# Kernel tuning notes

Hardware: AMD Instinct MI355X
Metric: run time of the kernel (lower is better)

## Reference

```python
import jax, jax.numpy as jnp
import numpy as np

BATCH = 2_000_000
IN_DIM = 10
OUT_DIM = 3


def setup_inputs() -> dict:
    key = jax.random.key(0)
    kx, kw, km = jax.random.split(key, 3)
    x = jax.random.normal(kx, (BATCH, IN_DIM), dtype=jnp.float32)
    W = jax.random.normal(kw, (OUT_DIM, IN_DIM), dtype=jnp.float32)
    # M initialized near identity (well-conditioned), matching torch.eye init
    M = jnp.eye(OUT_DIM, dtype=jnp.float32) + 0.1 * jax.random.normal(km, (OUT_DIM, OUT_DIM), dtype=jnp.float32)
    return {"x": x, "W": W, "M": M}


def reference(x, W, M):
    det_A = jnp.linalg.det(M)
    is_singular = jnp.isclose(det_A, jnp.float32(0.0))  # torch.isclose defaults: rtol=1e-5, atol=1e-8
    M_inv = jnp.linalg.inv(M)
    M_inv = jnp.where(is_singular, jnp.full_like(M_inv, jnp.nan), M_inv)
    # y = (M_inv @ W @ x.T).T == x @ (M_inv @ W).T
    proj = M_inv @ W                      # [out, in] tiny matmul
    return x @ proj.T                     # [batch, out]
```

## Files before the change

kernel.cpp:

```cpp
#include <hip/hip_runtime.h>

#define IN_DIM 10
#define OUT_DIM 3
#define BLOCK 256
#define ROWS_PER_BLOCK 512

__global__ __launch_bounds__(BLOCK) void simnet_fused(
    const float* __restrict__ x,
    const float* __restrict__ W,
    const float* __restrict__ M,
    float* __restrict__ out,
    long long batch)
{
    __shared__ float s_x[ROWS_PER_BLOCK * IN_DIM];
    __shared__ float s_proj[OUT_DIM * IN_DIM];

    const int t = threadIdx.x;
    const long long row0 = (long long)blockIdx.x * ROWS_PER_BLOCK;
    const long long total_in = batch * IN_DIM;

    if (t == 0) {
        const float a = M[0], b = M[1], c = M[2];
        const float d = M[3], e = M[4], f_ = M[5];
        const float g = M[6], h = M[7], i_ = M[8];
        const float A =  (e * i_ - f_ * h);
        const float B = -(d * i_ - f_ * g);
        const float C =  (d * h  - e  * g);
        const float det = a * A + b * B + c * C;
        float inv[3][3];
        if (fabsf(det) <= 1e-8f) {
            const float qn = __builtin_nanf("");
            #pragma unroll
            for (int o = 0; o < 3; ++o)
                #pragma unroll
                for (int k = 0; k < 3; ++k) inv[o][k] = qn;
        } else {
            const float r = 1.0f / det;
            inv[0][0] = A * r;
            inv[0][1] = (c * h  - b * i_) * r;
            inv[0][2] = (b * f_ - c * e ) * r;
            inv[1][0] = B * r;
            inv[1][1] = (a * i_ - c * g ) * r;
            inv[1][2] = (c * d  - a * f_) * r;
            inv[2][0] = C * r;
            inv[2][1] = (b * g  - a * h ) * r;
            inv[2][2] = (a * e  - b * d ) * r;
        }
        #pragma unroll
        for (int o = 0; o < OUT_DIM; ++o)
            #pragma unroll
            for (int j = 0; j < IN_DIM; ++j)
                s_proj[o * IN_DIM + j] = inv[o][0] * W[0 * IN_DIM + j]
                                       + inv[o][1] * W[1 * IN_DIM + j]
                                       + inv[o][2] * W[2 * IN_DIM + j];
    }

    {
        const long long base = row0 * IN_DIM;
        #pragma unroll
        for (int k = 0; k < 5; ++k) {
            const long long f = base + (long long)(k * BLOCK + t) * 4;
            float4 v = make_float4(0.f, 0.f, 0.f, 0.f);
            if (f + 4 <= total_in) {
                v = *reinterpret_cast<const float4*>(x + f);
            } else if (f < total_in) {
                const float* p = x + f;
                const int n = (int)(total_in - f);
                v.x = p[0];
                if (n > 1) v.y = p[1];
                if (n > 2) v.z = p[2];
            }
            *reinterpret_cast<float4*>(&s_x[(k * BLOCK + t) * 4]) = v;
        }
    }
    __syncthreads();

    float pj[OUT_DIM][IN_DIM];
    #pragma unroll
    for (int o = 0; o < OUT_DIM; ++o)
        #pragma unroll
        for (int j = 0; j < IN_DIM; ++j)
            pj[o][j] = s_proj[o * IN_DIM + j];

    float acc[2][OUT_DIM];
    #pragma unroll
    for (int r = 0; r < 2; ++r) {
        const int lr = t + r * BLOCK;
        float xv[IN_DIM];
        #pragma unroll
        for (int j = 0; j < IN_DIM; ++j) xv[j] = s_x[lr * IN_DIM + j];
        #pragma unroll
        for (int o = 0; o < OUT_DIM; ++o) {
            float s = 0.f;
            #pragma unroll
            for (int j = 0; j < IN_DIM; ++j) s = fmaf(xv[j], pj[o][j], s);
            acc[r][o] = s;
        }
    }
    __syncthreads();

    #pragma unroll
    for (int r = 0; r < 2; ++r) {
        const int lr = t + r * BLOCK;
        #pragma unroll
        for (int o = 0; o < OUT_DIM; ++o)
            s_x[lr * OUT_DIM + o] = acc[r][o];
    }
    __syncthreads();

    const long long out_base = row0 * OUT_DIM;
    const long long total_out = batch * OUT_DIM;
    #pragma unroll
    for (int k = 0; k < 2; ++k) {
        const int idx = k * BLOCK + t;
        if (idx < (ROWS_PER_BLOCK * OUT_DIM) / 4) {
            const long long f = out_base + (long long)idx * 4;
            if (f + 4 <= total_out) {
                *reinterpret_cast<float4*>(out + f) =
                    *reinterpret_cast<const float4*>(&s_x[idx * 4]);
            } else if (f < total_out) {
                const int n = (int)(total_out - f);
                for (int j = 0; j < n; ++j) out[f + j] = s_x[idx * 4 + j];
            }
        }
    }
}

extern "C" void kernel_launch(void* const* d_in, const int* in_sizes, int n_in,
                              void* d_out, int out_size, void* d_ws, size_t ws_size,
                              hipStream_t stream) {
    const float* x = (const float*)d_in[0];
    const float* W = (const float*)d_in[1];
    const float* M = (const float*)d_in[2];
    float* out = (float*)d_out;
    const long long batch = (long long)in_sizes[0] / IN_DIM;
    const int grid = (int)((batch + ROWS_PER_BLOCK - 1) / ROWS_PER_BLOCK);
    simnet_fused<<<grid, BLOCK, 0, stream>>>(x, W, M, out, batch);
}
```

Measured before the change: 24.23 us.

## Split projection setup into its own kernel and make streaming kernel wave-local

```diff
diff --git a/kernel.cpp b/kernel.cpp
--- a/kernel.cpp
+++ b/kernel.cpp
@@ -3,124 +3,132 @@
 #define IN_DIM 10
 #define OUT_DIM 3
 #define BLOCK 256
-#define ROWS_PER_BLOCK 512
+#define WPB 4
+#define RPW 128
 
-__global__ __launch_bounds__(BLOCK) void simnet_fused(
+__global__ void proj_setup_kernel(const float* __restrict__ W,
+                                  const float* __restrict__ M,
+                                  float* __restrict__ proj)
+{
+    const int t = threadIdx.x;
+    const float a = M[0], b = M[1], c = M[2];
+    const float d = M[3], e = M[4], f_ = M[5];
+    const float g = M[6], h = M[7], i_ = M[8];
+    const float A =  (e * i_ - f_ * h);
+    const float B = -(d * i_ - f_ * g);
+    const float C =  (d * h  - e  * g);
+    const float det = a * A + b * B + c * C;
+    float inv[3][3];
+    if (fabsf(det) <= 1e-8f) {
+        const float qn = __builtin_nanf("");
+        #pragma unroll
+        for (int o = 0; o < 3; ++o)
+            #pragma unroll
+            for (int k = 0; k < 3; ++k) inv[o][k] = qn;
+    } else {
+        const float r = 1.0f / det;
+        inv[0][0] = A * r;
+        inv[0][1] = (c * h  - b * i_) * r;
+        inv[0][2] = (b * f_ - c * e ) * r;
+        inv[1][0] = B * r;
+        inv[1][1] = (a * i_ - c * g ) * r;
+        inv[1][2] = (c * d  - a * f_) * r;
+        inv[2][0] = C * r;
+        inv[2][1] = (b * g  - a * h ) * r;
+        inv[2][2] = (a * e  - b * d ) * r;
+    }
+    if (t < OUT_DIM * IN_DIM) {
+        const int o = t / IN_DIM, j = t % IN_DIM;
+        proj[t] = inv[o][0] * W[0 * IN_DIM + j]
+                + inv[o][1] * W[1 * IN_DIM + j]
+                + inv[o][2] * W[2 * IN_DIM + j];
+    }
+}
+
+__global__ __launch_bounds__(BLOCK) void simnet_stream(
     const float* __restrict__ x,
-    const float* __restrict__ W,
-    const float* __restrict__ M,
+    const float* __restrict__ proj,
     float* __restrict__ out,
     long long batch)
 {
-    __shared__ float s_x[ROWS_PER_BLOCK * IN_DIM];
-    __shared__ float s_proj[OUT_DIM * IN_DIM];
+    __shared__ __align__(16) float s_in[WPB][RPW * IN_DIM];
 
-    const int t = threadIdx.x;
-    const long long row0 = (long long)blockIdx.x * ROWS_PER_BLOCK;
-    const long long total_in = batch * IN_DIM;
-
-    if (t == 0) {
-        const float a = M[0], b = M[1], c = M[2];
-        const float d = M[3], e = M[4], f_ = M[5];
-        const float g = M[6], h = M[7], i_ = M[8];
-        const float A =  (e * i_ - f_ * h);
-        const float B = -(d * i_ - f_ * g);
-        const float C =  (d * h  - e  * g);
-        const float det = a * A + b * B + c * C;
-        float inv[3][3];
-        if (fabsf(det) <= 1e-8f) {
-            const float qn = __builtin_nanf("");
-            #pragma unroll
-            for (int o = 0; o < 3; ++o)
-                #pragma unroll
-                for (int k = 0; k < 3; ++k) inv[o][k] = qn;
-        } else {
-            const float r = 1.0f / det;
-            inv[0][0] = A * r;
-            inv[0][1] = (c * h  - b * i_) * r;
-            inv[0][2] = (b * f_ - c * e ) * r;
-            inv[1][0] = B * r;
-            inv[1][1] = (a * i_ - c * g ) * r;
-            inv[1][2] = (c * d  - a * f_) * r;
-            inv[2][0] = C * r;
-            inv[2][1] = (b * g  - a * h ) * r;
-            inv[2][2] = (a * e  - b * d ) * r;
-        }
-        #pragma unroll
-        for (int o = 0; o < OUT_DIM; ++o)
-            #pragma unroll
-            for (int j = 0; j < IN_DIM; ++j)
-                s_proj[o * IN_DIM + j] = inv[o][0] * W[0 * IN_DIM + j]
-                                       + inv[o][1] * W[1 * IN_DIM + j]
-                                       + inv[o][2] * W[2 * IN_DIM + j];
-    }
-
-    {
-        const long long base = row0 * IN_DIM;
-        #pragma unroll
-        for (int k = 0; k < 5; ++k) {
-            const long long f = base + (long long)(k * BLOCK + t) * 4;
-            float4 v = make_float4(0.f, 0.f, 0.f, 0.f);
-            if (f + 4 <= total_in) {
-                v = *reinterpret_cast<const float4*>(x + f);
-            } else if (f < total_in) {
-                const float* p = x + f;
-                const int n = (int)(total_in - f);
-                v.x = p[0];
-                if (n > 1) v.y = p[1];
-                if (n > 2) v.z = p[2];
-            }
-            *reinterpret_cast<float4*>(&s_x[(k * BLOCK + t) * 4]) = v;
-        }
-    }
-    __syncthreads();
+    const int wv   = threadIdx.x >> 6;
+    const int lane = threadIdx.x & 63;
+    const long long tile = (long long)blockIdx.x * WPB + wv;
+    const long long row0 = tile * RPW;
+    if (row0 >= batch) return;
 
     float pj[OUT_DIM][IN_DIM];
     #pragma unroll
     for (int o = 0; o < OUT_DIM; ++o)
         #pragma unroll
         for (int j = 0; j < IN_DIM; ++j)
-            pj[o][j] = s_proj[o * IN_DIM + j];
+            pj[o][j] = proj[o * IN_DIM + j];
 
-    float acc[2][OUT_DIM];
-    #pragma unroll
-    for (int r = 0; r < 2; ++r) {
-        const int lr = t + r * BLOCK;
-        float xv[IN_DIM];
+    float* sin_ = s_in[wv];
+
+    if (row0 + RPW <= batch) {
+        const float4* src = reinterpret_cast<const float4*>(x + row0 * IN_DIM);
+        float4* dst = reinterpret_cast<float4*>(sin_);
         #pragma unroll
-        for (int j = 0; j < IN_DIM; ++j) xv[j] = s_x[lr * IN_DIM + j];
+        for (int k = 0; k < 5; ++k)
+            dst[k * 64 + lane] = src[k * 64 + lane];
+        asm volatile("s_waitcnt lgkmcnt(0)" ::: "memory");
+
+        float acc[2][OUT_DIM];
         #pragma unroll
-        for (int o = 0; o < OUT_DIM; ++o) {
-            float s = 0.f;
+        for (int r = 0; r < 2; ++r) {
+            const int lr = lane + r * 64;
+            const float2* s2 = reinterpret_cast<const float2*>(sin_ + lr * IN_DIM);
+            const float2 a0 = s2[0], a1 = s2[1], a2 = s2[2], a3 = s2[3], a4 = s2[4];
             #pragma unroll
-            for (int j = 0; j < IN_DIM; ++j) s = fmaf(xv[j], pj[o][j], s);
-            acc[r][o] = s;
+            for (int o = 0; o < OUT_DIM; ++o) {
+                float s;
+                s = a0.x * pj[o][0];
+                s = fmaf(a0.y, pj[o][1], s);
+                s = fmaf(a1.x, pj[o][2], s);
+                s = fmaf(a1.y, pj[o][3], s);
+                s = fmaf(a2.x, pj[o][4], s);
+                s = fmaf(a2.y, pj[o][5], s);
+                s = fmaf(a3.x, pj[o][6], s);
+                s = fmaf(a3.y, pj[o][7], s);
+                s = fmaf(a4.x, pj[o][8], s);
+                s = fmaf(a4.y, pj[o][9], s);
+                acc[r][o] = s;
+            }
         }
-    }
-    __syncthreads();
 
-    #pragma unroll
-    for (int r = 0; r < 2; ++r) {
-        const int lr = t + r * BLOCK;
         #pragma unroll
-        for (int o = 0; o < OUT_DIM; ++o)
-            s_x[lr * OUT_DIM + o] = acc[r][o];
-    }
-    __syncthreads();
+        for (int r = 0; r < 2; ++r) {
+            const int lr = lane + r * 64;
+            #pragma unroll
+            for (int o = 0; o < OUT_DIM; ++o)
+                sin_[lr * OUT_DIM + o] = acc[r][o];
+        }
+        asm volatile("s_waitcnt lgkmcnt(0)" ::: "memory");
 
-    const long long out_base = row0 * OUT_DIM;
-    const long long total_out = batch * OUT_DIM;
-    #pragma unroll
-    for (int k = 0; k < 2; ++k) {
-        const int idx = k * BLOCK + t;
-        if (idx < (ROWS_PER_BLOCK * OUT_DIM) / 4) {
-            const long long f = out_base + (long long)idx * 4;
-            if (f + 4 <= total_out) {
-                *reinterpret_cast<float4*>(out + f) =
-                    *reinterpret_cast<const float4*>(&s_x[idx * 4]);
-            } else if (f < total_out) {
-                const int n = (int)(total_out - f);
-                for (int j = 0; j < n; ++j) out[f + j] = s_x[idx * 4 + j];
+        float4* od = reinterpret_cast<float4*>(out + row0 * OUT_DIM);
+        const float4* so4 = reinterpret_cast<const float4*>(sin_);
+        od[lane] = so4[lane];
+        if (lane < 32) od[64 + lane] = so4[64 + lane];
+    } else {
+        #pragma unroll
+        for (int r = 0; r < 2; ++r) {
+            const long long row = row0 + lane + r * 64;
+            if (row < batch) {
+                float s0 = 0.f, s1 = 0.f, s2v = 0.f;
+                const float* xr = x + row * IN_DIM;
+                #pragma unroll
+                for (int j = 0; j < IN_DIM; ++j) {
+                    const float v = xr[j];
+                    s0  = fmaf(v, pj[0][j], s0);
+                    s1  = fmaf(v, pj[1][j], s1);
+                    s2v = fmaf(v, pj[2][j], s2v);
+                }
+                out[row * OUT_DIM + 0] = s0;
+                out[row * OUT_DIM + 1] = s1;
+                out[row * OUT_DIM + 2] = s2v;
             }
         }
     }
@@ -132,8 +140,13 @@
     const float* x = (const float*)d_in[0];
     const float* W = (const float*)d_in[1];
     const float* M = (const float*)d_in[2];
-    float* out = (float*)d_out;
+    float* out  = (float*)d_out;
+    float* proj = (float*)d_ws;
+
     const long long batch = (long long)in_sizes[0] / IN_DIM;
-    const int grid = (int)((batch + ROWS_PER_BLOCK - 1) / ROWS_PER_BLOCK);
-    simnet_fused<<<grid, BLOCK, 0, stream>>>(x, W, M, out, batch);
+    const long long n_tiles = (batch + RPW - 1) / RPW;
+    const int grid = (int)((n_tiles + WPB - 1) / WPB);
+
+    proj_setup_kernel<<<1, 64, 0, stream>>>(W, M, proj);
+    simnet_stream<<<grid, BLOCK, 0, stream>>>(x, proj, out, batch);
 }
```

After: 25.32 us. +4.5%, slower.

## Replace LDS-staged tiles with direct per-thread row-pair loads and stores

Applied to the files above, without the earlier changes.

```diff
diff --git a/kernel.cpp b/kernel.cpp
--- a/kernel.cpp
+++ b/kernel.cpp
@@ -3,126 +3,122 @@
 #define IN_DIM 10
 #define OUT_DIM 3
 #define BLOCK 256
-#define ROWS_PER_BLOCK 512
 
-__global__ __launch_bounds__(BLOCK) void simnet_fused(
+__global__ __launch_bounds__(BLOCK, 6) void simnet_direct(
     const float* __restrict__ x,
     const float* __restrict__ W,
     const float* __restrict__ M,
     float* __restrict__ out,
     long long batch)
 {
-    __shared__ float s_x[ROWS_PER_BLOCK * IN_DIM];
-    __shared__ float s_proj[OUT_DIM * IN_DIM];
+    const long long npairs = batch >> 1;
+    const long long p = (long long)blockIdx.x * BLOCK + threadIdx.x;
+    if (p >= npairs) return;
 
-    const int t = threadIdx.x;
-    const long long row0 = (long long)blockIdx.x * ROWS_PER_BLOCK;
-    const long long total_in = batch * IN_DIM;
+    const float4* xv = reinterpret_cast<const float4*>(x) + 5 * p;
+    const float4 v0 = xv[0];
+    const float4 v1 = xv[1];
+    const float4 v2 = xv[2];
+    const float4 v3 = xv[3];
+    const float4 v4 = xv[4];
 
-    if (t == 0) {
-        const float a = M[0], b = M[1], c = M[2];
-        const float d = M[3], e = M[4], f_ = M[5];
-        const float g = M[6], h = M[7], i_ = M[8];
-        const float A =  (e * i_ - f_ * h);
-        const float B = -(d * i_ - f_ * g);
-        const float C =  (d * h  - e  * g);
-        const float det = a * A + b * B + c * C;
-        float inv[3][3];
-        if (fabsf(det) <= 1e-8f) {
-            const float qn = __builtin_nanf("");
+    const float a = M[0], b = M[1], c = M[2];
+    const float d = M[3], e = M[4], f_ = M[5];
+    const float g = M[6], h = M[7], i_ = M[8];
+    const float A =  (e * i_ - f_ * h);
+    const float B = -(d * i_ - f_ * g);
+    const float C =  (d * h  - e  * g);
+    const float det = a * A + b * B + c * C;
+    float inv[3][3];
+    if (fabsf(det) <= 1e-8f) {
+        const float qn = __builtin_nanf("");
+        #pragma unroll
+        for (int o = 0; o < 3; ++o)
             #pragma unroll
-            for (int o = 0; o < 3; ++o)
-                #pragma unroll
-                for (int k = 0; k < 3; ++k) inv[o][k] = qn;
-        } else {
-            const float r = 1.0f / det;
-            inv[0][0] = A * r;
-            inv[0][1] = (c * h  - b * i_) * r;
-            inv[0][2] = (b * f_ - c * e ) * r;
-            inv[1][0] = B * r;
-            inv[1][1] = (a * i_ - c * g ) * r;
-            inv[1][2] = (c * d  - a * f_) * r;
-            inv[2][0] = C * r;
-            inv[2][1] = (b * g  - a * h ) * r;
-            inv[2][2] = (a * e  - b * d ) * r;
-        }
-        #pragma unroll
-        for (int o = 0; o < OUT_DIM; ++o)
-            #pragma unroll
-            for (int j = 0; j < IN_DIM; ++j)
-                s_proj[o * IN_DIM + j] = inv[o][0] * W[0 * IN_DIM + j]
-                                       + inv[o][1] * W[1 * IN_DIM + j]
-                                       + inv[o][2] * W[2 * IN_DIM + j];
+            for (int k = 0; k < 3; ++k) inv[o][k] = qn;
+    } else {
+        const float r = 1.0f / det;
+        inv[0][0] = A * r;
+        inv[0][1] = (c * h  - b * i_) * r;
+        inv[0][2] = (b * f_ - c * e ) * r;
+        inv[1][0] = B * r;
+        inv[1][1] = (a * i_ - c * g ) * r;
+        inv[1][2] = (c * d  - a * f_) * r;
+        inv[2][0] = C * r;
+        inv[2][1] = (b * g  - a * h ) * r;
+        inv[2][2] = (a * e  - b * d ) * r;
     }
-
-    {
-        const long long base = row0 * IN_DIM;
-        #pragma unroll
-        for (int k = 0; k < 5; ++k) {
-            const long long f = base + (long long)(k * BLOCK + t) * 4;
-            float4 v = make_float4(0.f, 0.f, 0.f, 0.f);
-            if (f + 4 <= total_in) {
-                v = *reinterpret_cast<const float4*>(x + f);
-            } else if (f < total_in) {
-                const float* p = x + f;
-                const int n = (int)(total_in - f);
-                v.x = p[0];
-                if (n > 1) v.y = p[1];
-                if (n > 2) v.z = p[2];
-            }
-            *reinterpret_cast<float4*>(&s_x[(k * BLOCK + t) * 4]) = v;
-        }
-    }
-    __syncthreads();
-
     float pj[OUT_DIM][IN_DIM];
     #pragma unroll
     for (int o = 0; o < OUT_DIM; ++o)
         #pragma unroll
         for (int j = 0; j < IN_DIM; ++j)
-            pj[o][j] = s_proj[o * IN_DIM + j];
+            pj[o][j] = inv[o][0] * W[0 * IN_DIM + j]
+                     + inv[o][1] * W[1 * IN_DIM + j]
+                     + inv[o][2] * W[2 * IN_DIM + j];
 
-    float acc[2][OUT_DIM];
+    const float r0j[IN_DIM] = { v0.x, v0.y, v0.z, v0.w,
+                                v1.x, v1.y, v1.z, v1.w,
+                                v2.x, v2.y };
+    const float r1j[IN_DIM] = { v2.z, v2.w,
+                                v3.x, v3.y, v3.z, v3.w,
+                                v4.x, v4.y, v4.z, v4.w };
+    float y0[OUT_DIM], y1[OUT_DIM];
     #pragma unroll
-    for (int r = 0; r < 2; ++r) {
-        const int lr = t + r * BLOCK;
-        float xv[IN_DIM];
+    for (int o = 0; o < OUT_DIM; ++o) {
+        float s0 = r0j[0] * pj[o][0];
+        float s1 = r1j[0] * pj[o][0];
         #pragma unroll
-        for (int j = 0; j < IN_DIM; ++j) xv[j] = s_x[lr * IN_DIM + j];
-        #pragma unroll
-        for (int o = 0; o < OUT_DIM; ++o) {
-            float s = 0.f;
-            #pragma unroll
-            for (int j = 0; j < IN_DIM; ++j) s = fmaf(xv[j], pj[o][j], s);
-            acc[r][o] = s;
+        for (int j = 1; j < IN_DIM; ++j) {
+            s0 = fmaf(r0j[j], pj[o][j], s0);
+            s1 = fmaf(r1j[j], pj[o][j], s1);
         }
+        y0[o] = s0;
+        y1[o] = s1;
     }
-    __syncthreads();
 
-    #pragma unroll
-    for (int r = 0; r < 2; ++r) {
-        const int lr = t + r * BLOCK;
-        #pragma unroll
-        for (int o = 0; o < OUT_DIM; ++o)
-            s_x[lr * OUT_DIM + o] = acc[r][o];
+    float2* o2 = reinterpret_cast<float2*>(out) + 3 * p;
+    o2[0] = make_float2(y0[0], y0[1]);
+    o2[1] = make_float2(y0[2], y1[0]);
+    o2[2] = make_float2(y1[1], y1[2]);
+}
+
+__global__ void simnet_tail(const float* __restrict__ x,
+                            const float* __restrict__ W,
+                            const float* __restrict__ M,
+                            float* __restrict__ out,
+                            long long batch)
+{
+    if (threadIdx.x != 0 || (batch & 1LL) == 0) return;
+    const long long row = batch - 1;
+    const float a = M[0], b = M[1], c = M[2];
+    const float d = M[3], e = M[4], f_ = M[5];
+    const float g = M[6], h = M[7], i_ = M[8];
+    const float A =  (e * i_ - f_ * h);
+    const float B = -(d * i_ - f_ * g);
+    const float C =  (d * h  - e  * g);
+    const float det = a * A + b * B + c * C;
+    float inv[3][3];
+    if (fabsf(det) <= 1e-8f) {
+        const float qn = __builtin_nanf("");
+        for (int o = 0; o < 3; ++o)
+            for (int k = 0; k < 3; ++k) inv[o][k] = qn;
+    } else {
+        const float r = 1.0f / det;
+        inv[0][0] = A * r;                  inv[0][1] = (c * h  - b * i_) * r;  inv[0][2] = (b * f_ - c * e ) * r;
+        inv[1][0] = B * r;                  inv[1][1] = (a * i_ - c * g ) * r;  inv[1][2] = (c * d  - a * f_) * r;
+        inv[2][0] = C * r;                  inv[2][1] = (b * g  - a * h ) * r;  inv[2][2] = (a * e  - b * d ) * r;
     }
-    __syncthreads();
-
-    const long long out_base = row0 * OUT_DIM;
-    const long long total_out = batch * OUT_DIM;
-    #pragma unroll
-    for (int k = 0; k < 2; ++k) {
-        const int idx = k * BLOCK + t;
-        if (idx < (ROWS_PER_BLOCK * OUT_DIM) / 4) {
-            const long long f = out_base + (long long)idx * 4;
-            if (f + 4 <= total_out) {
-                *reinterpret_cast<float4*>(out + f) =
-                    *reinterpret_cast<const float4*>(&s_x[idx * 4]);
-            } else if (f < total_out) {
-                const int n = (int)(total_out - f);
-                for (int j = 0; j < n; ++j) out[f + j] = s_x[idx * 4 + j];
-            }
+    const float* xr = x + row * IN_DIM;
+    for (int o = 0; o < OUT_DIM; ++o) {
+        float s = 0.f;
+        for (int j = 0; j < IN_DIM; ++j) {
+            const float pj = inv[o][0] * W[0 * IN_DIM + j]
+                           + inv[o][1] * W[1 * IN_DIM + j]
+                           + inv[o][2] * W[2 * IN_DIM + j];
+            s = fmaf(xr[j], pj, s);
         }
+        out[row * OUT_DIM + o] = s;
     }
 }
 
@@ -134,6 +130,9 @@
     const float* M = (const float*)d_in[2];
     float* out = (float*)d_out;
     const long long batch = (long long)in_sizes[0] / IN_DIM;
-    const int grid = (int)((batch + ROWS_PER_BLOCK - 1) / ROWS_PER_BLOCK);
-    simnet_fused<<<grid, BLOCK, 0, stream>>>(x, W, M, out, batch);
+    const long long npairs = batch >> 1;
+    const int grid = (int)((npairs + BLOCK - 1) / BLOCK);
+    simnet_direct<<<grid, BLOCK, 0, stream>>>(x, W, M, out, batch);
+    if (batch & 1LL)
+        simnet_tail<<<1, 64, 0, stream>>>(x, W, M, out, batch);
 }
```

Result: faster. 20.36 us (-16.0%).
